# Performance work log

Hardware: AMD Instinct MI355X
Metric: run time of the kernel (lower is better)

Reference implementation:

```python
import jax, jax.numpy as jnp
import numpy as np

FEATURE_DIM = 4
LOSS_WEIGHT = 1.0
DELTA_V = 0.5
DELTA_D = 1.5
NUM_LABELS = 8  # instance ids 0..7; 0 = background
B, H, W = 16, 640, 640


def _safe_norm(x, axis):
    # L2 norm with grad-safe sqrt (forward value exact: 0 when sum of squares is 0)
    sq = jnp.sum(x * x, axis=axis)
    pos = sq > 0
    return jnp.where(pos, jnp.sqrt(jnp.where(pos, sq, 1.0)), 0.0)


def _single_loss(emb, instance, kernel, training_mask):
    # emb: [H,W,C], instance: [H,W] int, kernel/training_mask: [H,W] float
    C = emb.shape[-1]
    L = NUM_LABELS
    tm = training_mask > 0.5
    kr = kernel > 0.5
    inst = jnp.where(tm, instance, 0).reshape(-1)          # [P]
    inst_k = jnp.where(kr.reshape(-1), inst, 0)            # [P]
    emb_f = emb.reshape(-1, C)                              # [P,C]

    # per-label kernel-region means (emb_mean), label 0 column is zeros
    sums = jax.ops.segment_sum(emb_f, inst_k, num_segments=L)                       # [L,C]
    cnts = jax.ops.segment_sum(jnp.ones(inst_k.shape, jnp.float32), inst_k, L)      # [L]
    mu = sums / jnp.maximum(cnts, 1.0)[:, None]
    mu = mu.at[0].set(0.0)

    # aggregation term: per-pixel distance to its instance mean
    d = _safe_norm(emb_f - mu[inst], axis=1)                                         # [P]
    term = jnp.log(jnp.maximum(d - DELTA_V, 0.0) ** 2 + 1.0)
    cnt_i = jax.ops.segment_sum(jnp.ones(inst.shape, jnp.float32), inst, L)
    agg = jax.ops.segment_sum(term, inst, L) / jnp.maximum(cnt_i, 1.0)               # [L]
    # original skips label 0, then takes mean of l_agg[1:] -> drops first nonzero label
    l_agg = jnp.mean(agg[2:])

    # discrimination term: all ordered pairs of distinct nonzero labels
    dd = _safe_norm(mu[:, None, :] - mu[None, :, :], axis=-1)                        # [L,L]
    valid = (1.0 - jnp.eye(L, dtype=jnp.float32)).at[0, :].set(0.0).at[:, 0].set(0.0)
    dis = jnp.log(jnp.maximum(2.0 * DELTA_D - dd, 0.0) ** 2 + 1.0)
    l_dis = jnp.sum(dis * valid) / jnp.sum(valid)

    l_reg = jnp.mean(jnp.log(_safe_norm(mu, axis=1) + 1.0)) * 0.001
    return l_agg + l_dis + l_reg


def reference(emb, instance, kernel, training_mask):
    losses = jax.vmap(_single_loss)(emb, instance, kernel, training_mask)  # [B]
    return LOSS_WEIGHT * jnp.mean(losses)


def setup_inputs() -> dict:
    key = jax.random.key(0)
    k1, k2, k3 = jax.random.split(key, 3)
    emb = jax.random.normal(k1, (B, H, W, FEATURE_DIM), dtype=jnp.float32)
    instance = jax.random.randint(k2, (B, H, W), 0, NUM_LABELS, dtype=jnp.int32)
    kernel = jax.random.uniform(k3, (B, H, W), dtype=jnp.float32)
    training_mask = jnp.ones((B, H, W), dtype=jnp.float32)
    return {"emb": emb, "instance": instance, "kernel": kernel, "training_mask": training_mask}
```

## Files before the change

kernel.cpp:

```cpp
#include <hip/hip_runtime.h>
#include <math.h>

#define NLAB 8
#define BATCH 16
#define S_OFF  0
#define CK_OFF 28
#define CI_OFF 35
#define AG_OFF 41
#define ACC_PER_B 48
#define ACC_FLOATS (BATCH * ACC_PER_B)
#define LAB_OFFSET 4096

__device__ __forceinline__ float wave_reduce(float v) {
#pragma unroll
  for (int off = 32; off > 0; off >>= 1) v += __shfl_xor(v, off, 64);
  return v;
}

__global__ __launch_bounds__(256, 4) void k_accum(
    const float4* __restrict__ emb, const int* __restrict__ inst,
    const float* __restrict__ ker, const float* __restrict__ tmk,
    float* __restrict__ acc, unsigned int* __restrict__ labc,
    int P, int use_cache)
{
  const int b = blockIdx.y;
  const size_t base = (size_t)b * P;
  const float4* e   = emb + base;
  const int4*   ip4 = (const int4*)(inst + base);
  const float4* kp4 = (const float4*)(ker + base);
  const float4* tp4 = (const float4*)(tmk + base);
  unsigned int* lb  = labc + (base >> 2);

  float s[7][4], ck[7], ci[6];
#pragma unroll
  for (int l = 0; l < 7; ++l) {
    ck[l] = 0.f;
    s[l][0] = 0.f; s[l][1] = 0.f; s[l][2] = 0.f; s[l][3] = 0.f;
  }
#pragma unroll
  for (int l = 0; l < 6; ++l) ci[l] = 0.f;

  const int nq = P >> 2;
  const int stride = blockDim.x * gridDim.x;

  for (int q = blockIdx.x * blockDim.x + threadIdx.x; q < nq; q += stride) {
    int4   iv = ip4[q];
    float4 kv = kp4[q];
    float4 tv = tp4[q];
    float4 e0 = e[4 * q + 0];
    float4 e1 = e[4 * q + 1];
    float4 e2 = e[4 * q + 2];
    float4 e3 = e[4 * q + 3];

    int lab0 = (tv.x > 0.5f) ? (iv.x & 7) : 0;
    int lab1 = (tv.y > 0.5f) ? (iv.y & 7) : 0;
    int lab2 = (tv.z > 0.5f) ? (iv.z & 7) : 0;
    int lab3 = (tv.w > 0.5f) ? (iv.w & 7) : 0;
    float k0 = (kv.x > 0.5f) ? 1.f : 0.f;
    float k1 = (kv.y > 0.5f) ? 1.f : 0.f;
    float k2 = (kv.z > 0.5f) ? 1.f : 0.f;
    float k3 = (kv.w > 0.5f) ? 1.f : 0.f;

    if (use_cache)
      lb[q] = (unsigned)lab0 | ((unsigned)lab1 << 8) |
              ((unsigned)lab2 << 16) | ((unsigned)lab3 << 24);

#pragma unroll
    for (int l = 1; l < NLAB; ++l) {
      float m0 = (lab0 == l) ? 1.f : 0.f;
      float m1 = (lab1 == l) ? 1.f : 0.f;
      float m2 = (lab2 == l) ? 1.f : 0.f;
      float m3 = (lab3 == l) ? 1.f : 0.f;
      float mk0 = m0 * k0, mk1 = m1 * k1, mk2 = m2 * k2, mk3 = m3 * k3;
      ck[l - 1] += (mk0 + mk1) + (mk2 + mk3);
      s[l - 1][0] = fmaf(mk0, e0.x, fmaf(mk1, e1.x, fmaf(mk2, e2.x, fmaf(mk3, e3.x, s[l - 1][0]))));
      s[l - 1][1] = fmaf(mk0, e0.y, fmaf(mk1, e1.y, fmaf(mk2, e2.y, fmaf(mk3, e3.y, s[l - 1][1]))));
      s[l - 1][2] = fmaf(mk0, e0.z, fmaf(mk1, e1.z, fmaf(mk2, e2.z, fmaf(mk3, e3.z, s[l - 1][2]))));
      s[l - 1][3] = fmaf(mk0, e0.w, fmaf(mk1, e1.w, fmaf(mk2, e2.w, fmaf(mk3, e3.w, s[l - 1][3]))));
      if (l >= 2) ci[l - 2] += (m0 + m1) + (m2 + m3);
    }
  }

  const int tail = P - (nq << 2);
  const int gtid = blockIdx.x * blockDim.x + threadIdx.x;
  if (gtid < tail) {
    int p = (nq << 2) + gtid;
    int lab = (tmk[base + p] > 0.5f) ? (inst[base + p] & 7) : 0;
    float kr = (ker[base + p] > 0.5f) ? 1.f : 0.f;
    float4 ev = e[p];
    if (use_cache)
      atomicAnd(&lb[p >> 2], ~(255u << (8 * (p & 3)))),
      atomicOr(&lb[p >> 2], (unsigned)lab << (8 * (p & 3)));
#pragma unroll
    for (int l = 1; l < NLAB; ++l) {
      float m = (lab == l) ? 1.f : 0.f;
      float mk = m * kr;
      ck[l - 1] += mk;
      s[l - 1][0] = fmaf(mk, ev.x, s[l - 1][0]);
      s[l - 1][1] = fmaf(mk, ev.y, s[l - 1][1]);
      s[l - 1][2] = fmaf(mk, ev.z, s[l - 1][2]);
      s[l - 1][3] = fmaf(mk, ev.w, s[l - 1][3]);
      if (l >= 2) ci[l - 2] += m;
    }
  }

  __shared__ float red[4][48];
  const int wid = threadIdx.x >> 6, lane = threadIdx.x & 63;
#pragma unroll
  for (int l = 0; l < 7; ++l) {
#pragma unroll
    for (int c = 0; c < 4; ++c) {
      float v = wave_reduce(s[l][c]);
      if (lane == 0) red[wid][S_OFF + l * 4 + c] = v;
    }
    float vk = wave_reduce(ck[l]);
    if (lane == 0) red[wid][CK_OFF + l] = vk;
  }
#pragma unroll
  for (int l = 0; l < 6; ++l) {
    float vi = wave_reduce(ci[l]);
    if (lane == 0) red[wid][CI_OFF + l] = vi;
  }
  __syncthreads();
  if (threadIdx.x < AG_OFF) {
    float v = red[0][threadIdx.x] + red[1][threadIdx.x] +
              red[2][threadIdx.x] + red[3][threadIdx.x];
    atomicAdd(acc + b * ACC_PER_B + threadIdx.x, v);
  }
}

__global__ __launch_bounds__(256, 4) void k_agg(
    const float4* __restrict__ emb, const int* __restrict__ inst,
    const float* __restrict__ tmk, const unsigned int* __restrict__ labc,
    float* __restrict__ acc, int P, int use_cache)
{
  const int b = blockIdx.y;
  const size_t base = (size_t)b * P;
  __shared__ float4 smu[NLAB];
  const float* accB = acc + b * ACC_PER_B;
  if (threadIdx.x < NLAB) {
    int l = threadIdx.x;
    float4 m;
    if (l == 0) {
      m = make_float4(0.f, 0.f, 0.f, 0.f);
    } else {
      float inv = 1.f / fmaxf(accB[CK_OFF + l - 1], 1.f);
      m = make_float4(accB[S_OFF + (l - 1) * 4 + 0] * inv,
                      accB[S_OFF + (l - 1) * 4 + 1] * inv,
                      accB[S_OFF + (l - 1) * 4 + 2] * inv,
                      accB[S_OFF + (l - 1) * 4 + 3] * inv);
    }
    smu[l] = m;
  }
  __syncthreads();

  const float4* e = emb + base;
  const unsigned int* lb = labc + (base >> 2);
  const int4*   ip4 = (const int4*)(inst + base);
  const float4* tp4 = (const float4*)(tmk + base);

  float aggl[6];
#pragma unroll
  for (int l = 0; l < 6; ++l) aggl[l] = 0.f;

  const int nq = P >> 2;
  const int stride = blockDim.x * gridDim.x;

  for (int q = blockIdx.x * blockDim.x + threadIdx.x; q < nq; q += stride) {
    int lab0, lab1, lab2, lab3;
    if (use_cache) {
      unsigned lu = lb[q];
      lab0 = lu & 255; lab1 = (lu >> 8) & 255;
      lab2 = (lu >> 16) & 255; lab3 = (lu >> 24) & 255;
    } else {
      int4 iv = ip4[q]; float4 tv = tp4[q];
      lab0 = (tv.x > 0.5f) ? (iv.x & 7) : 0;
      lab1 = (tv.y > 0.5f) ? (iv.y & 7) : 0;
      lab2 = (tv.z > 0.5f) ? (iv.z & 7) : 0;
      lab3 = (tv.w > 0.5f) ? (iv.w & 7) : 0;
    }
    float4 e0 = e[4 * q + 0];
    float4 e1 = e[4 * q + 1];
    float4 e2 = e[4 * q + 2];
    float4 e3 = e[4 * q + 3];

#pragma unroll
    for (int i = 0; i < 4; ++i) {
      int lab = (i == 0) ? lab0 : (i == 1) ? lab1 : (i == 2) ? lab2 : lab3;
      float4 ev = (i == 0) ? e0 : (i == 1) ? e1 : (i == 2) ? e2 : e3;
      float4 mv = smu[lab];
      float dx = ev.x - mv.x, dy = ev.y - mv.y;
      float dz = ev.z - mv.z, dw = ev.w - mv.w;
      float sq = dx * dx + dy * dy + dz * dz + dw * dw;
      float d = sqrtf(sq);
      float t = fmaxf(d - 0.5f, 0.f);
      float term = (lab >= 2) ? logf(fmaf(t, t, 1.f)) : 0.f;
#pragma unroll
      for (int l = 0; l < 6; ++l) aggl[l] += (lab == l + 2) ? term : 0.f;
    }
  }

  const int tail = P - (nq << 2);
  const int gtid = blockIdx.x * blockDim.x + threadIdx.x;
  if (gtid < tail) {
    int p = (nq << 2) + gtid;
    int lab = (tmk[base + p] > 0.5f) ? (inst[base + p] & 7) : 0;
    float4 ev = e[p];
    float4 mv = smu[lab];
    float dx = ev.x - mv.x, dy = ev.y - mv.y;
    float dz = ev.z - mv.z, dw = ev.w - mv.w;
    float d = sqrtf(dx * dx + dy * dy + dz * dz + dw * dw);
    float t = fmaxf(d - 0.5f, 0.f);
    float term = (lab >= 2) ? logf(fmaf(t, t, 1.f)) : 0.f;
#pragma unroll
    for (int l = 0; l < 6; ++l) aggl[l] += (lab == l + 2) ? term : 0.f;
  }

  __shared__ float red[4][8];
  const int wid = threadIdx.x >> 6, lane = threadIdx.x & 63;
#pragma unroll
  for (int l = 0; l < 6; ++l) {
    float v = wave_reduce(aggl[l]);
    if (lane == 0) red[wid][l] = v;
  }
  __syncthreads();
  if (threadIdx.x < 6) {
    float v = red[0][threadIdx.x] + red[1][threadIdx.x] +
              red[2][threadIdx.x] + red[3][threadIdx.x];
    atomicAdd(acc + b * ACC_PER_B + AG_OFF + threadIdx.x, v);
  }
}

__global__ void k_final(const float* __restrict__ acc, float* __restrict__ out, int nb) {
  const int lane = threadIdx.x;
  float loss = 0.f;
  if (lane < nb) {
    const float* a = acc + lane * ACC_PER_B;
    float mu[NLAB][4];
#pragma unroll
    for (int c = 0; c < 4; ++c) mu[0][c] = 0.f;
#pragma unroll
    for (int l = 1; l < NLAB; ++l) {
      float inv = 1.f / fmaxf(a[CK_OFF + l - 1], 1.f);
#pragma unroll
      for (int c = 0; c < 4; ++c) mu[l][c] = a[S_OFF + (l - 1) * 4 + c] * inv;
    }
    float l_agg = 0.f;
#pragma unroll
    for (int l = 2; l < NLAB; ++l)
      l_agg += a[AG_OFF + l - 2] / fmaxf(a[CI_OFF + l - 2], 1.f);
    l_agg *= (1.f / 6.f);
    float ssum = 0.f;
    for (int i = 1; i < NLAB; ++i)
      for (int j = 1; j < NLAB; ++j) {
        if (i == j) continue;
        float dx = mu[i][0] - mu[j][0], dy = mu[i][1] - mu[j][1];
        float dz = mu[i][2] - mu[j][2], dw = mu[i][3] - mu[j][3];
        float dd = sqrtf(dx * dx + dy * dy + dz * dz + dw * dw);
        float t = fmaxf(3.0f - dd, 0.f);
        ssum += logf(fmaf(t, t, 1.f));
      }
    float l_dis = ssum / 42.f;
    float rsum = 0.f;
#pragma unroll
    for (int l = 1; l < NLAB; ++l) {
      float n = sqrtf(mu[l][0] * mu[l][0] + mu[l][1] * mu[l][1] +
                      mu[l][2] * mu[l][2] + mu[l][3] * mu[l][3]);
      rsum += logf(n + 1.f);
    }
    float l_reg = rsum * (0.001f / NLAB);
    loss = l_agg + l_dis + l_reg;
  }
  loss = wave_reduce(loss);
  if (lane == 0) out[0] = loss / (float)nb;
}

extern "C" void kernel_launch(void* const* d_in, const int* in_sizes, int n_in,
                              void* d_out, int out_size, void* d_ws, size_t ws_size,
                              hipStream_t stream) {
  const float4* emb = (const float4*)d_in[0];
  const int*    inst = (const int*)d_in[1];
  const float*  ker  = (const float*)d_in[2];
  const float*  tmk  = (const float*)d_in[3];
  float* out = (float*)d_out;

  const int total = in_sizes[1];
  const int P = total / BATCH;

  float* acc = (float*)d_ws;
  unsigned int* labc = (unsigned int*)((char*)d_ws + LAB_OFFSET);
  const size_t need = (size_t)LAB_OFFSET + (size_t)total;
  const int use_cache = (ws_size >= need && (P & 3) == 0) ? 1 : 0;

  hipMemsetAsync(d_ws, 0, ACC_FLOATS * sizeof(float), stream);

  dim3 grid(128, BATCH);
  k_accum<<<grid, 256, 0, stream>>>(emb, inst, ker, tmk, acc, labc, P, use_cache);
  k_agg  <<<grid, 256, 0, stream>>>(emb, inst, tmk, labc, acc, P, use_cache);
  k_final<<<1, 64, 0, stream>>>(acc, out, BATCH);
}
```

Measured before the change: 249.3 us.

## Switch to strided per-pixel access with byte label cache and larger grid

Each thread now handles four pixels spaced a full grid-stride apart instead of four contiguous ones. Label, kernel and mask reads become scalar coalesced loads, embedding reads become consecutive float4 loads per lane, and the label cache is written and read one byte per pixel. This drops the separate tail path and the P%4 requirement for the cache, and raises the grid from 128 to 200 blocks per batch. The aim is better coalescing and more memory parallelism. The cost is narrower per-thread loads (scalar instead of int4/float4 for the label inputs) and byte-sized stores to the cache.

```diff
diff --git a/kernel.cpp b/kernel.cpp
--- a/kernel.cpp
+++ b/kernel.cpp
@@ -10,6 +10,7 @@
 #define ACC_PER_B 48
 #define ACC_FLOATS (BATCH * ACC_PER_B)
 #define LAB_OFFSET 4096
+#define GRIDX 200
 
 __device__ __forceinline__ float wave_reduce(float v) {
 #pragma unroll
@@ -20,16 +21,16 @@
 __global__ __launch_bounds__(256, 4) void k_accum(
     const float4* __restrict__ emb, const int* __restrict__ inst,
     const float* __restrict__ ker, const float* __restrict__ tmk,
-    float* __restrict__ acc, unsigned int* __restrict__ labc,
+    float* __restrict__ acc, unsigned char* __restrict__ labc,
     int P, int use_cache)
 {
   const int b = blockIdx.y;
   const size_t base = (size_t)b * P;
-  const float4* e   = emb + base;
-  const int4*   ip4 = (const int4*)(inst + base);
-  const float4* kp4 = (const float4*)(ker + base);
-  const float4* tp4 = (const float4*)(tmk + base);
-  unsigned int* lb  = labc + (base >> 2);
+  const float4* e  = emb + base;
+  const int*    ip = inst + base;
+  const float*  kp = ker + base;
+  const float*  tp = tmk + base;
+  unsigned char* lb = labc + base;
 
   float s[7][4], ck[7], ci[6];
 #pragma unroll
@@ -40,30 +41,34 @@
 #pragma unroll
   for (int l = 0; l < 6; ++l) ci[l] = 0.f;
 
-  const int nq = P >> 2;
-  const int stride = blockDim.x * gridDim.x;
-
-  for (int q = blockIdx.x * blockDim.x + threadIdx.x; q < nq; q += stride) {
-    int4   iv = ip4[q];
-    float4 kv = kp4[q];
-    float4 tv = tp4[q];
-    float4 e0 = e[4 * q + 0];
-    float4 e1 = e[4 * q + 1];
-    float4 e2 = e[4 * q + 2];
-    float4 e3 = e[4 * q + 3];
-
-    int lab0 = (tv.x > 0.5f) ? (iv.x & 7) : 0;
-    int lab1 = (tv.y > 0.5f) ? (iv.y & 7) : 0;
-    int lab2 = (tv.z > 0.5f) ? (iv.z & 7) : 0;
-    int lab3 = (tv.w > 0.5f) ? (iv.w & 7) : 0;
-    float k0 = (kv.x > 0.5f) ? 1.f : 0.f;
-    float k1 = (kv.y > 0.5f) ? 1.f : 0.f;
-    float k2 = (kv.z > 0.5f) ? 1.f : 0.f;
-    float k3 = (kv.w > 0.5f) ? 1.f : 0.f;
-
-    if (use_cache)
-      lb[q] = (unsigned)lab0 | ((unsigned)lab1 << 8) |
-              ((unsigned)lab2 << 16) | ((unsigned)lab3 << 24);
+  const int T   = blockDim.x * gridDim.x;
+  const int tid = blockIdx.x * blockDim.x + threadIdx.x;
+
+  for (int p0 = tid; p0 < P; p0 += 4 * T) {
+    const int p1 = p0 + T, p2 = p0 + 2 * T, p3 = p0 + 3 * T;
+    const bool v1 = p1 < P, v2 = p2 < P, v3 = p3 < P;
+    const int q1 = v1 ? p1 : p0, q2 = v2 ? p2 : p0, q3 = v3 ? p3 : p0;
+
+    int   i0 = ip[p0], i1 = ip[q1], i2 = ip[q2], i3 = ip[q3];
+    float t0v = tp[p0], t1v = tp[q1], t2v = tp[q2], t3v = tp[q3];
+    float c0v = kp[p0], c1v = kp[q1], c2v = kp[q2], c3v = kp[q3];
+    float4 e0 = e[p0], e1 = e[q1], e2 = e[q2], e3 = e[q3];
+
+    int lab0 = (t0v > 0.5f)       ? (i0 & 7) : 0;
+    int lab1 = (v1 && t1v > 0.5f) ? (i1 & 7) : 0;
+    int lab2 = (v2 && t2v > 0.5f) ? (i2 & 7) : 0;
+    int lab3 = (v3 && t3v > 0.5f) ? (i3 & 7) : 0;
+    float k0 = (c0v > 0.5f) ? 1.f : 0.f;
+    float k1 = (c1v > 0.5f) ? 1.f : 0.f;
+    float k2 = (c2v > 0.5f) ? 1.f : 0.f;
+    float k3 = (c3v > 0.5f) ? 1.f : 0.f;
+
+    if (use_cache) {
+      lb[p0] = (unsigned char)lab0;
+      if (v1) lb[p1] = (unsigned char)lab1;
+      if (v2) lb[p2] = (unsigned char)lab2;
+      if (v3) lb[p3] = (unsigned char)lab3;
+    }
 
 #pragma unroll
     for (int l = 1; l < NLAB; ++l) {
@@ -81,29 +86,6 @@
     }
   }
 
-  const int tail = P - (nq << 2);
-  const int gtid = blockIdx.x * blockDim.x + threadIdx.x;
-  if (gtid < tail) {
-    int p = (nq << 2) + gtid;
-    int lab = (tmk[base + p] > 0.5f) ? (inst[base + p] & 7) : 0;
-    float kr = (ker[base + p] > 0.5f) ? 1.f : 0.f;
-    float4 ev = e[p];
-    if (use_cache)
-      atomicAnd(&lb[p >> 2], ~(255u << (8 * (p & 3)))),
-      atomicOr(&lb[p >> 2], (unsigned)lab << (8 * (p & 3)));
-#pragma unroll
-    for (int l = 1; l < NLAB; ++l) {
-      float m = (lab == l) ? 1.f : 0.f;
-      float mk = m * kr;
-      ck[l - 1] += mk;
-      s[l - 1][0] = fmaf(mk, ev.x, s[l - 1][0]);
-      s[l - 1][1] = fmaf(mk, ev.y, s[l - 1][1]);
-      s[l - 1][2] = fmaf(mk, ev.z, s[l - 1][2]);
-      s[l - 1][3] = fmaf(mk, ev.w, s[l - 1][3]);
-      if (l >= 2) ci[l - 2] += m;
-    }
-  }
-
   __shared__ float red[4][48];
   const int wid = threadIdx.x >> 6, lane = threadIdx.x & 63;
 #pragma unroll
@@ -131,7 +113,7 @@
 
 __global__ __launch_bounds__(256, 4) void k_agg(
     const float4* __restrict__ emb, const int* __restrict__ inst,
-    const float* __restrict__ tmk, const unsigned int* __restrict__ labc,
+    const float* __restrict__ tmk, const unsigned char* __restrict__ labc,
     float* __restrict__ acc, int P, int use_cache)
 {
   const int b = blockIdx.y;
@@ -155,34 +137,37 @@
   __syncthreads();
 
   const float4* e = emb + base;
-  const unsigned int* lb = labc + (base >> 2);
-  const int4*   ip4 = (const int4*)(inst + base);
-  const float4* tp4 = (const float4*)(tmk + base);
+  const unsigned char* lb = labc + base;
+  const int*   ip = inst + base;
+  const float* tp = tmk + base;
 
   float aggl[6];
 #pragma unroll
   for (int l = 0; l < 6; ++l) aggl[l] = 0.f;
 
-  const int nq = P >> 2;
-  const int stride = blockDim.x * gridDim.x;
-
-  for (int q = blockIdx.x * blockDim.x + threadIdx.x; q < nq; q += stride) {
+  const int T   = blockDim.x * gridDim.x;
+  const int tid = blockIdx.x * blockDim.x + threadIdx.x;
+
+  for (int p0 = tid; p0 < P; p0 += 4 * T) {
+    const int p1 = p0 + T, p2 = p0 + 2 * T, p3 = p0 + 3 * T;
+    const bool v1 = p1 < P, v2 = p2 < P, v3 = p3 < P;
+    const int q1 = v1 ? p1 : p0, q2 = v2 ? p2 : p0, q3 = v3 ? p3 : p0;
+
     int lab0, lab1, lab2, lab3;
     if (use_cache) {
-      unsigned lu = lb[q];
-      lab0 = lu & 255; lab1 = (lu >> 8) & 255;
-      lab2 = (lu >> 16) & 255; lab3 = (lu >> 24) & 255;
+      lab0 = lb[p0];
+      lab1 = v1 ? lb[p1] : 0;
+      lab2 = v2 ? lb[p2] : 0;
+      lab3 = v3 ? lb[p3] : 0;
     } else {
-      int4 iv = ip4[q]; float4 tv = tp4[q];
-      lab0 = (tv.x > 0.5f) ? (iv.x & 7) : 0;
-      lab1 = (tv.y > 0.5f) ? (iv.y & 7) : 0;
-      lab2 = (tv.z > 0.5f) ? (iv.z & 7) : 0;
-      lab3 = (tv.w > 0.5f) ? (iv.w & 7) : 0;
-    }
-    float4 e0 = e[4 * q + 0];
-    float4 e1 = e[4 * q + 1];
-    float4 e2 = e[4 * q + 2];
-    float4 e3 = e[4 * q + 3];
+      int   i0 = ip[p0], i1 = ip[q1], i2 = ip[q2], i3 = ip[q3];
+      float t0v = tp[p0], t1v = tp[q1], t2v = tp[q2], t3v = tp[q3];
+      lab0 = (t0v > 0.5f)       ? (i0 & 7) : 0;
+      lab1 = (v1 && t1v > 0.5f) ? (i1 & 7) : 0;
+      lab2 = (v2 && t2v > 0.5f) ? (i2 & 7) : 0;
+      lab3 = (v3 && t3v > 0.5f) ? (i3 & 7) : 0;
+    }
+    float4 e0 = e[p0], e1 = e[q1], e2 = e[q2], e3 = e[q3];
 
 #pragma unroll
     for (int i = 0; i < 4; ++i) {
@@ -198,22 +183,6 @@
 #pragma unroll
       for (int l = 0; l < 6; ++l) aggl[l] += (lab == l + 2) ? term : 0.f;
     }
-  }
-
-  const int tail = P - (nq << 2);
-  const int gtid = blockIdx.x * blockDim.x + threadIdx.x;
-  if (gtid < tail) {
-    int p = (nq << 2) + gtid;
-    int lab = (tmk[base + p] > 0.5f) ? (inst[base + p] & 7) : 0;
-    float4 ev = e[p];
-    float4 mv = smu[lab];
-    float dx = ev.x - mv.x, dy = ev.y - mv.y;
-    float dz = ev.z - mv.z, dw = ev.w - mv.w;
-    float d = sqrtf(dx * dx + dy * dy + dz * dz + dw * dw);
-    float t = fmaxf(d - 0.5f, 0.f);
-    float term = (lab >= 2) ? logf(fmaf(t, t, 1.f)) : 0.f;
-#pragma unroll
-    for (int l = 0; l < 6; ++l) aggl[l] += (lab == l + 2) ? term : 0.f;
   }
 
   __shared__ float red[4][8];
@@ -288,13 +257,13 @@
   const int P = total / BATCH;
 
   float* acc = (float*)d_ws;
-  unsigned int* labc = (unsigned int*)((char*)d_ws + LAB_OFFSET);
+  unsigned char* labc = (unsigned char*)((char*)d_ws + LAB_OFFSET);
   const size_t need = (size_t)LAB_OFFSET + (size_t)total;
-  const int use_cache = (ws_size >= need && (P & 3) == 0) ? 1 : 0;
+  const int use_cache = (ws_size >= need) ? 1 : 0;
 
   hipMemsetAsync(d_ws, 0, ACC_FLOATS * sizeof(float), stream);
 
-  dim3 grid(128, BATCH);
+  dim3 grid(GRIDX, BATCH);
   k_accum<<<grid, 256, 0, stream>>>(emb, inst, ker, tmk, acc, labc, P, use_cache);
   k_agg  <<<grid, 256, 0, stream>>>(emb, inst, tmk, labc, acc, P, use_cache);
   k_final<<<1, 64, 0, stream>>>(acc, out, BATCH);
```

Result: no change. 246.5 us (-1.1%).
